# Optimization experiments

Hardware: AMD Instinct MI355X
Metric: run time of the kernel (lower is better)

Reference implementation:

```python
import jax, jax.numpy as jnp
import numpy as np

B, T, D, H = 512, 256, 64, 64  # batch, seq_len, input_dim, hidden_dim


def _lstm_params(key, in_dim, hid):
    k = 1.0 / np.sqrt(hid)
    k1, k2, k3, k4 = jax.random.split(key, 4)
    W_ih = jax.random.uniform(k1, (4 * hid, in_dim), jnp.float32, -k, k)
    W_hh = jax.random.uniform(k2, (4 * hid, hid), jnp.float32, -k, k)
    b_ih = jax.random.uniform(k3, (4 * hid,), jnp.float32, -k, k)
    b_hh = jax.random.uniform(k4, (4 * hid,), jnp.float32, -k, k)
    return W_ih, W_hh, b_ih, b_hh


def setup_inputs() -> dict:
    key = jax.random.key(0)
    ks = jax.random.split(key, 5)
    inp = {"x": jax.random.normal(ks[0], (B, T, D), jnp.float32)}
    names = ["enc0", "enc1", "dec0", "dec1"]
    # encoder: D->H, H->H ; decoder: H->D, D->D (decoder hidden size = input_dim)
    dims = [(D, H), (H, H), (H, D), (D, D)]
    for name, (i, h), k in zip(names, dims, ks[1:]):
        W_ih, W_hh, b_ih, b_hh = _lstm_params(k, i, h)
        inp[f"{name}_Wih"] = W_ih
        inp[f"{name}_Whh"] = W_hh
        inp[f"{name}_bih"] = b_ih
        inp[f"{name}_bhh"] = b_hh
    return inp


def lstm_layer(x, W_ih, W_hh, b_ih, b_hh):
    # x: [B, T, in]; PyTorch gate order: i, f, g, o
    b = x.shape[0]
    h_dim = W_hh.shape[1]
    # precompute input contribution for all timesteps (one big GEMM)
    xg = jnp.einsum('bti,gi->btg', x, W_ih) + b_ih + b_hh  # [B, T, 4H]

    def step(carry, xt):
        h, c = carry
        g = xt + h @ W_hh.T  # [B, 4H]
        i, f, gg, o = jnp.split(g, 4, axis=-1)
        i = jax.nn.sigmoid(i)
        f = jax.nn.sigmoid(f)
        gg = jnp.tanh(gg)
        o = jax.nn.sigmoid(o)
        c = f * c + i * gg
        h = o * jnp.tanh(c)
        return (h, c), h

    h0 = jnp.zeros((b, h_dim), x.dtype)
    (_, _), hs = jax.lax.scan(step, (h0, h0), jnp.swapaxes(xg, 0, 1))
    return jnp.swapaxes(hs, 0, 1)  # [B, T, H]


def reference(x,
              enc0_Wih, enc0_Whh, enc0_bih, enc0_bhh,
              enc1_Wih, enc1_Whh, enc1_bih, enc1_bhh,
              dec0_Wih, dec0_Whh, dec0_bih, dec0_bhh,
              dec1_Wih, dec1_Whh, dec1_bih, dec1_bhh):
    # Eval-mode forward (inter-layer dropout p=0.2 is disabled at inference)
    h = lstm_layer(x, enc0_Wih, enc0_Whh, enc0_bih, enc0_bhh)
    enc = lstm_layer(h, enc1_Wih, enc1_Whh, enc1_bih, enc1_bhh)
    h = lstm_layer(enc, dec0_Wih, dec0_Whh, dec0_bih, dec0_bhh)
    dec = lstm_layer(h, dec1_Wih, dec1_Whh, dec1_bih, dec1_bhh)
    return dec
```

## Files before the change

kernel.cpp:

```cpp
#include <hip/hip_runtime.h>


typedef _Float16 f16x8 __attribute__((ext_vector_type(8)));
typedef float    f32x4 __attribute__((ext_vector_type(4)));

#define TSEQ 256

__device__ __forceinline__ float fast_rcp(float x) { return __builtin_amdgcn_rcpf(x); }
__device__ __forceinline__ float sigm(float x) { return fast_rcp(1.0f + __expf(-x)); }
__device__ __forceinline__ float tanh_fast(float x) {
    return 2.0f * fast_rcp(1.0f + __expf(-2.0f * x)) - 1.0f;
}
__device__ __forceinline__ f16x8 cvt8(float4 a, float4 b) {
    f16x8 f;
    f[0] = (_Float16)a.x; f[1] = (_Float16)a.y; f[2] = (_Float16)a.z; f[3] = (_Float16)a.w;
    f[4] = (_Float16)b.x; f[5] = (_Float16)b.y; f[6] = (_Float16)b.z; f[7] = (_Float16)b.w;
    return f;
}
__device__ __forceinline__ float bperm(int addr, float v) {
    return __int_as_float(__builtin_amdgcn_ds_bpermute(addr, __float_as_int(v)));
}

__global__ __launch_bounds__(512, 2)
void lstm_fused11(const float* __restrict__ x,
                  float* __restrict__ out,
                  const float* __restrict__ Wih0, const float* __restrict__ Whh0,
                  const float* __restrict__ bi0,  const float* __restrict__ bh0,
                  const float* __restrict__ Wih1, const float* __restrict__ Whh1,
                  const float* __restrict__ bi1,  const float* __restrict__ bh1,
                  const float* __restrict__ Wih2, const float* __restrict__ Whh2,
                  const float* __restrict__ bi2,  const float* __restrict__ bh2,
                  const float* __restrict__ Wih3, const float* __restrict__ Whh3,
                  const float* __restrict__ bi3,  const float* __restrict__ bh3)
{
    __shared__ _Float16 Hb[2][4][2][64];

    const int tid  = threadIdx.x;
    const int wave = tid >> 6;
    const int lane = tid & 63;
    const int L    = wave >> 1;
    const int mh   = wave & 1;
    const int q    = lane >> 4;
    const int n    = lane & 15;
    const int b0   = blockIdx.x * 2;

    const float* Wih = (L == 0) ? Wih0 : (L == 1) ? Wih1 : (L == 2) ? Wih2 : Wih3;
    const float* Whh = (L == 0) ? Whh0 : (L == 1) ? Whh1 : (L == 2) ? Whh2 : Whh3;
    const float* bi  = (L == 0) ? bi0  : (L == 1) ? bi1  : (L == 2) ? bi2  : bi3;
    const float* bh  = (L == 0) ? bh0  : (L == 1) ? bh1  : (L == 2) ? bh2  : bh3;

    f16x8 Bih[4][2][2], Bhh[4][2][2];
#pragma unroll
    for (int g = 0; g < 4; ++g) {
#pragma unroll
        for (int s = 0; s < 2; ++s) {
            const int row = g * 64 + mh * 32 + s * 16 + n;
#pragma unroll
            for (int c = 0; c < 2; ++c) {
                const float* pi = Wih + row * 64 + c * 32 + q * 8;
                const float* ph = Whh + row * 64 + c * 32 + q * 8;
                f16x8 fi, fh;
#pragma unroll
                for (int k = 0; k < 8; ++k) { fi[k] = (_Float16)pi[k]; fh[k] = (_Float16)ph[k]; }
                Bih[g][s][c] = fi;
                Bhh[g][s][c] = fh;
            }
        }
    }

    const int eu = lane & 31;
    const int el = lane >> 5;
    const int unit = mh * 32 + eu;
    float4 be;
    be.x = bi[unit]       + bh[unit];
    be.y = bi[64 + unit]  + bh[64 + unit];
    be.z = bi[128 + unit] + bh[128 + unit];
    be.w = bi[192 + unit] + bh[192 + unit];
    float cst = 0.0f;
    float* outp = out + ((size_t)(b0 + el) * TSEQ) * 64 + unit;

    const int baddr = n * 4;

    ((int*)Hb)[tid] = 0;

    const float* xbase = x + ((size_t)(b0 + (n & 1)) * TSEQ) * 64 + q * 8;
    float4 R0, R1, R2, R3;
    R0 = R1 = R2 = R3 = make_float4(0.f, 0.f, 0.f, 0.f);
    if (L == 0 && n < 2) {
        R0 = *(const float4*)(xbase);      R1 = *(const float4*)(xbase + 4);
        R2 = *(const float4*)(xbase + 32); R3 = *(const float4*)(xbase + 36);
    }

    __syncthreads();

    for (int tau = 0; tau < TSEQ + 3; ++tau) {
        const int  t   = tau - L;
        const bool act = (unsigned)t < TSEQ;
        const int  pr  = (tau + 1) & 1;
        const int  pw  = tau & 1;

        if (act) {
            f16x8 vf0, vf1;
            if (L == 0) {
                vf0 = cvt8(R0, R1);
                vf1 = cvt8(R2, R3);
                if (t + 1 < TSEQ && n < 2) {
                    const float* p = xbase + (size_t)(t + 1) * 64;
                    R0 = *(const float4*)(p);      R1 = *(const float4*)(p + 4);
                    R2 = *(const float4*)(p + 32); R3 = *(const float4*)(p + 36);
                }
            } else {
                const _Float16* vp = &Hb[pr][L - 1][n & 1][0];
                vf0 = *(const f16x8*)(vp + q * 8);
                vf1 = *(const f16x8*)(vp + 32 + q * 8);
            }
            const _Float16* hp = &Hb[pr][L][n & 1][0];
            f16x8 hf0 = *(const f16x8*)(hp + q * 8);
            f16x8 hf1 = *(const f16x8*)(hp + 32 + q * 8);

            const f32x4 z4 = {0.f, 0.f, 0.f, 0.f};

            f32x4 Cgs[2][4];
#pragma unroll
            for (int s = 0; s < 2; ++s) {
#pragma unroll
                for (int g = 0; g < 4; ++g) {
                    f32x4 c;
                    c = __builtin_amdgcn_mfma_f32_16x16x32_f16(hf0, Bhh[g][s][0], z4, 0, 0, 0);
                    c = __builtin_amdgcn_mfma_f32_16x16x32_f16(hf1, Bhh[g][s][1], c,  0, 0, 0);
                    c = __builtin_amdgcn_mfma_f32_16x16x32_f16(vf0, Bih[g][s][0], c,  0, 0, 0);
                    Cgs[s][g] = __builtin_amdgcn_mfma_f32_16x16x32_f16(vf1, Bih[g][s][1], c, 0, 0, 0);
                }
            }

            float gv[4];
#pragma unroll
            for (int g = 0; g < 4; ++g) {
                float v00 = bperm(baddr, Cgs[0][g][0]);
                float v10 = bperm(baddr, Cgs[1][g][0]);
                float v01 = bperm(baddr, Cgs[0][g][1]);
                float v11 = bperm(baddr, Cgs[1][g][1]);
                float lo = (q & 1) ? v10 : v00;
                float hi = (q & 1) ? v11 : v01;
                gv[g] = (q & 2) ? hi : lo;
            }

            float gi = sigm(gv[0] + be.x);
            float gf = sigm(gv[1] + be.y);
            float gg = tanh_fast(gv[2] + be.z);
            float go = sigm(gv[3] + be.w);
            cst = gf * cst + gi * gg;
            float h = go * tanh_fast(cst);

            if (L == 3) outp[(size_t)t * 64] = h;
            Hb[pw][L][el][unit] = (_Float16)h;
        }
        __builtin_amdgcn_sched_barrier(0);
        asm volatile("s_waitcnt lgkmcnt(0)" ::: "memory");
        __builtin_amdgcn_s_barrier();
        __builtin_amdgcn_sched_barrier(0);
    }
}

extern "C" void kernel_launch(void* const* d_in, const int* in_sizes, int n_in,
                              void* d_out, int out_size, void* d_ws, size_t ws_size,
                              hipStream_t stream) {
    const float* x = (const float*)d_in[0];
    float* out = (float*)d_out;

    lstm_fused11<<<256, 512, 0, stream>>>(
        x, out,
        (const float*)d_in[1],  (const float*)d_in[2],
        (const float*)d_in[3],  (const float*)d_in[4],
        (const float*)d_in[5],  (const float*)d_in[6],
        (const float*)d_in[7],  (const float*)d_in[8],
        (const float*)d_in[9],  (const float*)d_in[10],
        (const float*)d_in[11], (const float*)d_in[12],
        (const float*)d_in[13], (const float*)d_in[14],
        (const float*)d_in[15], (const float*)d_in[16]);
}
```

Measured before the change: 383.5 us.

## Process two timesteps per block barrier using pairwise wave spin-flag sync

Each loop iteration now handles two consecutive timesteps per layer. The mid-iteration dependency between the two waves of a layer is handled by a shared-memory flag spin-wait rather than a full block barrier. The hidden-state buffer grows to four slots and x prefetch is doubled to match. This halves the number of block-wide barriers, at the cost of busy-wait polling with s_sleep, extra registers, and a correctness risk if the flag ordering or slot reuse is wrong.

```diff
diff --git a/kernel.cpp b/kernel.cpp
--- a/kernel.cpp
+++ b/kernel.cpp
@@ -22,7 +22,7 @@
 }
 
 __global__ __launch_bounds__(512, 2)
-void lstm_fused11(const float* __restrict__ x,
+void lstm_fused12(const float* __restrict__ x,
                   float* __restrict__ out,
                   const float* __restrict__ Wih0, const float* __restrict__ Whh0,
                   const float* __restrict__ bi0,  const float* __restrict__ bh0,
@@ -33,7 +33,8 @@
                   const float* __restrict__ Wih3, const float* __restrict__ Whh3,
                   const float* __restrict__ bi3,  const float* __restrict__ bh3)
 {
-    __shared__ _Float16 Hb[2][4][2][64];
+    __shared__ _Float16 Hb[4][4][2][64];
+    __shared__ int      Sf[8];
 
     const int tid  = threadIdx.x;
     const int wave = tid >> 6;
@@ -82,43 +83,55 @@
     const int baddr = n * 4;
 
     ((int*)Hb)[tid] = 0;
+    ((int*)Hb)[tid + 512] = 0;
+    if (tid < 8) Sf[tid] = -2;
 
     const float* xbase = x + ((size_t)(b0 + (n & 1)) * TSEQ) * 64 + q * 8;
-    float4 R0, R1, R2, R3;
-    R0 = R1 = R2 = R3 = make_float4(0.f, 0.f, 0.f, 0.f);
+    float4 A0, A1, A2, A3, B0, B1, B2, B3;
+    A0 = A1 = A2 = A3 = make_float4(0.f, 0.f, 0.f, 0.f);
+    B0 = B1 = B2 = B3 = A0;
     if (L == 0 && n < 2) {
-        R0 = *(const float4*)(xbase);      R1 = *(const float4*)(xbase + 4);
-        R2 = *(const float4*)(xbase + 32); R3 = *(const float4*)(xbase + 36);
+        A0 = *(const float4*)(xbase);      A1 = *(const float4*)(xbase + 4);
+        A2 = *(const float4*)(xbase + 32); A3 = *(const float4*)(xbase + 36);
+        B0 = *(const float4*)(xbase + 64);  B1 = *(const float4*)(xbase + 68);
+        B2 = *(const float4*)(xbase + 96);  B3 = *(const float4*)(xbase + 100);
     }
 
     __syncthreads();
 
-    for (int tau = 0; tau < TSEQ + 3; ++tau) {
-        const int  t   = tau - L;
-        const bool act = (unsigned)t < TSEQ;
-        const int  pr  = (tau + 1) & 1;
-        const int  pw  = tau & 1;
-
+    const f32x4 z4 = {0.f, 0.f, 0.f, 0.f};
+    const int NI = 131;
+
+    for (int i = 0; i < NI; ++i) {
+        const bool act = (unsigned)(i - L) < 128u;
         if (act) {
-            f16x8 vf0, vf1;
+            const int s0 = 2 * (i - L);
+            const int s1 = s0 + 1;
+
+            f16x8 vfA0, vfA1, vfB0, vfB1;
             if (L == 0) {
-                vf0 = cvt8(R0, R1);
-                vf1 = cvt8(R2, R3);
-                if (t + 1 < TSEQ && n < 2) {
-                    const float* p = xbase + (size_t)(t + 1) * 64;
-                    R0 = *(const float4*)(p);      R1 = *(const float4*)(p + 4);
-                    R2 = *(const float4*)(p + 32); R3 = *(const float4*)(p + 36);
+                vfA0 = cvt8(A0, A1);  vfA1 = cvt8(A2, A3);
+                vfB0 = cvt8(B0, B1);  vfB1 = cvt8(B2, B3);
+                if (s0 + 2 < TSEQ && n < 2) {
+                    const float* p = xbase + (size_t)(s0 + 2) * 64;
+                    A0 = *(const float4*)(p);      A1 = *(const float4*)(p + 4);
+                    A2 = *(const float4*)(p + 32); A3 = *(const float4*)(p + 36);
+                    if (s0 + 3 < TSEQ) {
+                        B0 = *(const float4*)(p + 64); B1 = *(const float4*)(p + 68);
+                        B2 = *(const float4*)(p + 96); B3 = *(const float4*)(p + 100);
+                    }
                 }
             } else {
-                const _Float16* vp = &Hb[pr][L - 1][n & 1][0];
-                vf0 = *(const f16x8*)(vp + q * 8);
-                vf1 = *(const f16x8*)(vp + 32 + q * 8);
-            }
-            const _Float16* hp = &Hb[pr][L][n & 1][0];
+                const _Float16* va = &Hb[s0 & 3][L - 1][n & 1][0];
+                vfA0 = *(const f16x8*)(va + q * 8);
+                vfA1 = *(const f16x8*)(va + 32 + q * 8);
+                const _Float16* vb = &Hb[s1 & 3][L - 1][n & 1][0];
+                vfB0 = *(const f16x8*)(vb + q * 8);
+                vfB1 = *(const f16x8*)(vb + 32 + q * 8);
+            }
+            const _Float16* hp = &Hb[(s0 - 1) & 3][L][n & 1][0];
             f16x8 hf0 = *(const f16x8*)(hp + q * 8);
             f16x8 hf1 = *(const f16x8*)(hp + 32 + q * 8);
-
-            const f32x4 z4 = {0.f, 0.f, 0.f, 0.f};
 
             f32x4 Cgs[2][4];
 #pragma unroll
@@ -128,11 +141,10 @@
                     f32x4 c;
                     c = __builtin_amdgcn_mfma_f32_16x16x32_f16(hf0, Bhh[g][s][0], z4, 0, 0, 0);
                     c = __builtin_amdgcn_mfma_f32_16x16x32_f16(hf1, Bhh[g][s][1], c,  0, 0, 0);
-                    c = __builtin_amdgcn_mfma_f32_16x16x32_f16(vf0, Bih[g][s][0], c,  0, 0, 0);
-                    Cgs[s][g] = __builtin_amdgcn_mfma_f32_16x16x32_f16(vf1, Bih[g][s][1], c, 0, 0, 0);
+                    c = __builtin_amdgcn_mfma_f32_16x16x32_f16(vfA0, Bih[g][s][0], c,  0, 0, 0);
+                    Cgs[s][g] = __builtin_amdgcn_mfma_f32_16x16x32_f16(vfA1, Bih[g][s][1], c, 0, 0, 0);
                 }
             }
-
             float gv[4];
 #pragma unroll
             for (int g = 0; g < 4; ++g) {
@@ -144,16 +156,60 @@
                 float hi = (q & 1) ? v11 : v01;
                 gv[g] = (q & 2) ? hi : lo;
             }
-
-            float gi = sigm(gv[0] + be.x);
-            float gf = sigm(gv[1] + be.y);
-            float gg = tanh_fast(gv[2] + be.z);
-            float go = sigm(gv[3] + be.w);
-            cst = gf * cst + gi * gg;
-            float h = go * tanh_fast(cst);
-
-            if (L == 3) outp[(size_t)t * 64] = h;
-            Hb[pw][L][el][unit] = (_Float16)h;
+            {
+                float gi = sigm(gv[0] + be.x);
+                float gf = sigm(gv[1] + be.y);
+                float gg = tanh_fast(gv[2] + be.z);
+                float go = sigm(gv[3] + be.w);
+                cst = gf * cst + gi * gg;
+                float h = go * tanh_fast(cst);
+                if (L == 3) outp[(size_t)s0 * 64] = h;
+                Hb[s0 & 3][L][el][unit] = (_Float16)h;
+            }
+
+            asm volatile("s_waitcnt lgkmcnt(0)" ::: "memory");
+            if (lane == 0) ((volatile int*)Sf)[wave] = s0;
+            for (;;) {
+                asm volatile("" ::: "memory");
+                int pv = ((volatile int*)Sf)[wave ^ 1];
+                if (pv >= s0) break;
+                __builtin_amdgcn_s_sleep(1);
+            }
+            const _Float16* hq = &Hb[s0 & 3][L][n & 1][0];
+            f16x8 hg0 = *(const f16x8*)(hq + q * 8);
+            f16x8 hg1 = *(const f16x8*)(hq + 32 + q * 8);
+
+#pragma unroll
+            for (int s = 0; s < 2; ++s) {
+#pragma unroll
+                for (int g = 0; g < 4; ++g) {
+                    f32x4 c;
+                    c = __builtin_amdgcn_mfma_f32_16x16x32_f16(hg0, Bhh[g][s][0], z4, 0, 0, 0);
+                    c = __builtin_amdgcn_mfma_f32_16x16x32_f16(hg1, Bhh[g][s][1], c,  0, 0, 0);
+                    c = __builtin_amdgcn_mfma_f32_16x16x32_f16(vfB0, Bih[g][s][0], c,  0, 0, 0);
+                    Cgs[s][g] = __builtin_amdgcn_mfma_f32_16x16x32_f16(vfB1, Bih[g][s][1], c, 0, 0, 0);
+                }
+            }
+#pragma unroll
+            for (int g = 0; g < 4; ++g) {
+                float v00 = bperm(baddr, Cgs[0][g][0]);
+                float v10 = bperm(baddr, Cgs[1][g][0]);
+                float v01 = bperm(baddr, Cgs[0][g][1]);
+                float v11 = bperm(baddr, Cgs[1][g][1]);
+                float lo = (q & 1) ? v10 : v00;
+                float hi = (q & 1) ? v11 : v01;
+                gv[g] = (q & 2) ? hi : lo;
+            }
+            {
+                float gi = sigm(gv[0] + be.x);
+                float gf = sigm(gv[1] + be.y);
+                float gg = tanh_fast(gv[2] + be.z);
+                float go = sigm(gv[3] + be.w);
+                cst = gf * cst + gi * gg;
+                float h = go * tanh_fast(cst);
+                if (L == 3) outp[(size_t)s1 * 64] = h;
+                Hb[s1 & 3][L][el][unit] = (_Float16)h;
+            }
         }
         __builtin_amdgcn_sched_barrier(0);
         asm volatile("s_waitcnt lgkmcnt(0)" ::: "memory");
@@ -168,7 +224,7 @@
     const float* x = (const float*)d_in[0];
     float* out = (float*)d_out;
 
-    lstm_fused11<<<256, 512, 0, stream>>>(
+    lstm_fused12<<<256, 512, 0, stream>>>(
         x, out,
         (const float*)d_in[1],  (const float*)d_in[2],
         (const float*)d_in[3],  (const float*)d_in[4],
```

Result: no change. 385.4 us (+0.5%).

## Batch four timesteps per block barrier with intra-layer wave-pair flag sync

Applied to the files above, without the earlier changes.

Processes four timesteps per outer iteration. The input projection for all four steps is computed up front in one MFMA batch by packing the steps into different rows of the 16-row tile. Within a layer, the two waves now coordinate through LDS spin-wait flags instead of a full block barrier each step, so the block-wide barrier runs once per four steps. The history buffer grows to 8 slots per layer to hold these results. This cuts barrier count and latency on the serial recurrence, at the cost of spin-wait polling, more LDS, and more complex indexing that could hide ordering bugs.

```diff
diff --git a/kernel.cpp b/kernel.cpp
--- a/kernel.cpp
+++ b/kernel.cpp
@@ -22,7 +22,7 @@
 }
 
 __global__ __launch_bounds__(512, 2)
-void lstm_fused11(const float* __restrict__ x,
+void lstm_fused14(const float* __restrict__ x,
                   float* __restrict__ out,
                   const float* __restrict__ Wih0, const float* __restrict__ Whh0,
                   const float* __restrict__ bi0,  const float* __restrict__ bh0,
@@ -33,7 +33,8 @@
                   const float* __restrict__ Wih3, const float* __restrict__ Whh3,
                   const float* __restrict__ bi3,  const float* __restrict__ bh3)
 {
-    __shared__ _Float16 Hb[2][4][2][64];
+    __shared__ _Float16 Hb[4][8][2][72];
+    __shared__ int      Sf[8];
 
     const int tid  = threadIdx.x;
     const int wave = tid >> 6;
@@ -42,6 +43,7 @@
     const int mh   = wave & 1;
     const int q    = lane >> 4;
     const int n    = lane & 15;
+    const int stp  = (n >> 1) & 3;
     const int b0   = blockIdx.x * 2;
 
     const float* Wih = (L == 0) ? Wih0 : (L == 1) ? Wih1 : (L == 2) ? Wih2 : Wih3;
@@ -79,46 +81,102 @@
     float cst = 0.0f;
     float* outp = out + ((size_t)(b0 + el) * TSEQ) * 64 + unit;
 
-    const int baddr = n * 4;
-
-    ((int*)Hb)[tid] = 0;
+    for (int iz = tid; iz < 2304; iz += 512) ((int*)Hb)[iz] = 0;
+    if (tid < 8) Sf[tid] = -2;
 
     const float* xbase = x + ((size_t)(b0 + (n & 1)) * TSEQ) * 64 + q * 8;
     float4 R0, R1, R2, R3;
     R0 = R1 = R2 = R3 = make_float4(0.f, 0.f, 0.f, 0.f);
-    if (L == 0 && n < 2) {
-        R0 = *(const float4*)(xbase);      R1 = *(const float4*)(xbase + 4);
-        R2 = *(const float4*)(xbase + 32); R3 = *(const float4*)(xbase + 36);
+    if (L == 0 && n < 8) {
+        const float* p = xbase + (size_t)stp * 64;
+        R0 = *(const float4*)(p);      R1 = *(const float4*)(p + 4);
+        R2 = *(const float4*)(p + 32); R3 = *(const float4*)(p + 36);
     }
 
     __syncthreads();
 
-    for (int tau = 0; tau < TSEQ + 3; ++tau) {
-        const int  t   = tau - L;
-        const bool act = (unsigned)t < TSEQ;
-        const int  pr  = (tau + 1) & 1;
-        const int  pw  = tau & 1;
-
+    const f32x4 z4 = {0.f, 0.f, 0.f, 0.f};
+    const int NI = 67;
+
+#define DO_STEP(J, R0I, R1I, QS)                                              \
+    {                                                                         \
+        if ((J) > 0) {                                                        \
+            const int need = s0 + (J) - 1;                                    \
+            for (;;) {                                                        \
+                asm volatile("" ::: "memory");                                \
+                int pv = ((volatile int*)Sf)[wave ^ 1];                       \
+                if (pv >= need) break;                                        \
+                __builtin_amdgcn_s_sleep(1);                                  \
+            }                                                                 \
+        }                                                                     \
+        f16x8 hf0, hf1;                                                       \
+        _Pragma("unroll")                                                     \
+        for (int k = 0; k < 8; ++k) { hf0[k] = (_Float16)0.f; hf1[k] = (_Float16)0.f; } \
+        if (stp == (J)) {                                                     \
+            const _Float16* hp = &Hb[L][(s0 + (J) - 1) & 7][n & 1][0];        \
+            hf0 = *(const f16x8*)(hp + q * 8);                                \
+            hf1 = *(const f16x8*)(hp + 32 + q * 8);                           \
+        }                                                                     \
+        _Pragma("unroll")                                                     \
+        for (int s = 0; s < 2; ++s) {                                         \
+            _Pragma("unroll")                                                 \
+            for (int g = 0; g < 4; ++g) {                                     \
+                f32x4 c;                                                      \
+                c = __builtin_amdgcn_mfma_f32_16x16x32_f16(hf0, Bhh[g][s][0], Cgs[s][g], 0, 0, 0); \
+                Cgs[s][g] = __builtin_amdgcn_mfma_f32_16x16x32_f16(hf1, Bhh[g][s][1], c, 0, 0, 0); \
+            }                                                                 \
+        }                                                                     \
+        const int ba = (((QS) << 4) + n) * 4;                                 \
+        float gv[4];                                                          \
+        _Pragma("unroll")                                                     \
+        for (int g = 0; g < 4; ++g) {                                         \
+            float v00 = bperm(ba, Cgs[0][g][R0I]);                            \
+            float v10 = bperm(ba, Cgs[1][g][R0I]);                            \
+            float v01 = bperm(ba, Cgs[0][g][R1I]);                            \
+            float v11 = bperm(ba, Cgs[1][g][R1I]);                            \
+            float lo = (q & 1) ? v10 : v00;                                   \
+            float hi = (q & 1) ? v11 : v01;                                   \
+            gv[g] = (q & 2) ? hi : lo;                                        \
+        }                                                                     \
+        {                                                                     \
+            float gi = sigm(gv[0] + be.x);                                    \
+            float gf = sigm(gv[1] + be.y);                                    \
+            float gg = tanh_fast(gv[2] + be.z);                               \
+            float go = sigm(gv[3] + be.w);                                    \
+            cst = gf * cst + gi * gg;                                         \
+            float h = go * tanh_fast(cst);                                    \
+            if (L == 3) outp[(size_t)(s0 + (J)) * 64] = h;                    \
+            Hb[L][(s0 + (J)) & 7][el][unit] = (_Float16)h;                    \
+        }                                                                     \
+        if ((J) < 3) {                                                        \
+            asm volatile("s_waitcnt lgkmcnt(0)" ::: "memory");                \
+            if (lane == 0) ((volatile int*)Sf)[wave] = s0 + (J);              \
+        }                                                                     \
+    }
+
+    for (int i = 0; i < NI; ++i) {
+        const bool act = (unsigned)(i - L) < 64u;
         if (act) {
+            const int s0 = 4 * (i - L);
+            const int g0 = s0 & 7;
+
             f16x8 vf0, vf1;
             if (L == 0) {
                 vf0 = cvt8(R0, R1);
                 vf1 = cvt8(R2, R3);
-                if (t + 1 < TSEQ && n < 2) {
-                    const float* p = xbase + (size_t)(t + 1) * 64;
-                    R0 = *(const float4*)(p);      R1 = *(const float4*)(p + 4);
-                    R2 = *(const float4*)(p + 32); R3 = *(const float4*)(p + 36);
+                if (n < 8) {
+                    const int tl = s0 + 4 + stp;
+                    if (tl < TSEQ) {
+                        const float* p = xbase + (size_t)tl * 64;
+                        R0 = *(const float4*)(p);      R1 = *(const float4*)(p + 4);
+                        R2 = *(const float4*)(p + 32); R3 = *(const float4*)(p + 36);
+                    }
                 }
             } else {
-                const _Float16* vp = &Hb[pr][L - 1][n & 1][0];
+                const _Float16* vp = &Hb[L - 1][g0 + stp][n & 1][0];
                 vf0 = *(const f16x8*)(vp + q * 8);
                 vf1 = *(const f16x8*)(vp + 32 + q * 8);
             }
-            const _Float16* hp = &Hb[pr][L][n & 1][0];
-            f16x8 hf0 = *(const f16x8*)(hp + q * 8);
-            f16x8 hf1 = *(const f16x8*)(hp + 32 + q * 8);
-
-            const f32x4 z4 = {0.f, 0.f, 0.f, 0.f};
 
             f32x4 Cgs[2][4];
 #pragma unroll
@@ -126,40 +184,22 @@
 #pragma unroll
                 for (int g = 0; g < 4; ++g) {
                     f32x4 c;
-                    c = __builtin_amdgcn_mfma_f32_16x16x32_f16(hf0, Bhh[g][s][0], z4, 0, 0, 0);
-                    c = __builtin_amdgcn_mfma_f32_16x16x32_f16(hf1, Bhh[g][s][1], c,  0, 0, 0);
-                    c = __builtin_amdgcn_mfma_f32_16x16x32_f16(vf0, Bih[g][s][0], c,  0, 0, 0);
+                    c = __builtin_amdgcn_mfma_f32_16x16x32_f16(vf0, Bih[g][s][0], z4, 0, 0, 0);
                     Cgs[s][g] = __builtin_amdgcn_mfma_f32_16x16x32_f16(vf1, Bih[g][s][1], c, 0, 0, 0);
                 }
             }
 
-            float gv[4];
-#pragma unroll
-            for (int g = 0; g < 4; ++g) {
-                float v00 = bperm(baddr, Cgs[0][g][0]);
-                float v10 = bperm(baddr, Cgs[1][g][0]);
-                float v01 = bperm(baddr, Cgs[0][g][1]);
-                float v11 = bperm(baddr, Cgs[1][g][1]);
-                float lo = (q & 1) ? v10 : v00;
-                float hi = (q & 1) ? v11 : v01;
-                gv[g] = (q & 2) ? hi : lo;
-            }
-
-            float gi = sigm(gv[0] + be.x);
-            float gf = sigm(gv[1] + be.y);
-            float gg = tanh_fast(gv[2] + be.z);
-            float go = sigm(gv[3] + be.w);
-            cst = gf * cst + gi * gg;
-            float h = go * tanh_fast(cst);
-
-            if (L == 3) outp[(size_t)t * 64] = h;
-            Hb[pw][L][el][unit] = (_Float16)h;
+            DO_STEP(0, 0, 1, 0)
+            DO_STEP(1, 2, 3, 0)
+            DO_STEP(2, 0, 1, 1)
+            DO_STEP(3, 2, 3, 1)
         }
         __builtin_amdgcn_sched_barrier(0);
         asm volatile("s_waitcnt lgkmcnt(0)" ::: "memory");
         __builtin_amdgcn_s_barrier();
         __builtin_amdgcn_sched_barrier(0);
     }
+#undef DO_STEP
 }
 
 extern "C" void kernel_launch(void* const* d_in, const int* in_sizes, int n_in,
@@ -168,7 +208,7 @@
     const float* x = (const float*)d_in[0];
     float* out = (float*)d_out;
 
-    lstm_fused11<<<256, 512, 0, stream>>>(
+    lstm_fused14<<<256, 512, 0, stream>>>(
         x, out,
         (const float*)d_in[1],  (const float*)d_in[2],
         (const float*)d_in[3],  (const float*)d_in[4],
```

Measured after the change: 325.4 us. 1.18x faster.
